# Kernel tuning notes

Measured on AMD Instinct MI355X. Metric: run time of the kernel, lower is better.

## Reference

```python
import jax, jax.numpy as jnp
import numpy as np

N = 8192          # total genes
B = 16            # number of ragged batch groups (equal-size here: 512 each)
D = 768           # hidden_dim
NEG = -1.0e9      # mask fill value used by the original module


def setup_inputs() -> dict:
    key = jax.random.key(0)
    ks = jax.random.split(key, 10)
    s = 0.02
    inp = {
        "gene_embeddings": jax.random.normal(ks[0], (N, D), dtype=jnp.float32),
        # sorted group ids: 16 contiguous groups of 512 genes
        "batch": (jnp.arange(N) // (N // B)).astype(jnp.int64),
        "Wq": jax.random.normal(ks[1], (D, D), dtype=jnp.float32) * s,
        "bq": jnp.zeros((D,), dtype=jnp.float32),
        "Wk": jax.random.normal(ks[2], (D, D), dtype=jnp.float32) * s,
        "bk": jnp.zeros((D,), dtype=jnp.float32),
        "Wv": jax.random.normal(ks[3], (D, D), dtype=jnp.float32) * s,
        "bv": jnp.zeros((D,), dtype=jnp.float32),
        "Wo": jax.random.normal(ks[4], (D, D), dtype=jnp.float32) * s,
        "bo": jnp.zeros((D,), dtype=jnp.float32),
        "beta": jnp.ones((1,), dtype=jnp.float32) * 0.1,
    }
    return inp


def reference(gene_embeddings, batch, Wq, bq, Wk, bk, Wv, bv, Wo, bo, beta):
    # Single-head attention over full hidden_dim (num_heads unused in original).
    x = gene_embeddings
    q = x @ Wq.T + bq                      # [N, D]
    k = x @ Wk.T + bk
    v = x @ Wv.T + bv
    scale = 1.0 / jnp.sqrt(jnp.asarray(D, dtype=x.dtype))
    scores = (q @ k.T) * scale             # [N, N]
    # block-diagonal group mask + diagonal self-mask (same -1e9 fill as torch code)
    same_group = batch[:, None] == batch[None, :]
    eye = jnp.eye(N, dtype=bool)
    allow = same_group & (~eye)
    scores = jnp.where(allow, scores, NEG)
    weights = jax.nn.softmax(scores, axis=-1)   # dropout in eval mode -> identity
    dyn = weights @ v                       # [N, D]
    dyn = dyn @ Wo.T + bo
    return x + beta * dyn
```

## Files before the change

kernel.cpp:

```cpp
#include <hip/hip_runtime.h>
#include <hip/hip_bf16.h>
#include <cstdint>

using u16 = unsigned short;
using u32 = unsigned int;

typedef __bf16 bf16x8 __attribute__((ext_vector_type(8)));
typedef float  f32x4  __attribute__((ext_vector_type(4)));

__device__ __forceinline__ u32 f2b2(float a, float b) {
    __hip_bfloat162 h = __float22bfloat162_rn(float2{a, b});
    u32 u;
    __builtin_memcpy(&u, &h, 4);
    return u;
}
__device__ __forceinline__ float b2f(u16 b) {
    u32 u = (u32)b << 16;
    float f;
    __builtin_memcpy(&f, &u, 4);
    return f;
}

__device__ __forceinline__ void gload_lds16(const u16* g, u16* l) {
    __builtin_amdgcn_global_load_lds(
        (const __attribute__((address_space(1))) void*)g,
        (__attribute__((address_space(3))) void*)l,
        16, 0, 0);
}

#define VMCNT(N)  asm volatile("s_waitcnt vmcnt(" #N ")" ::: "memory")
#define LGKMCNT0  asm volatile("s_waitcnt lgkmcnt(0)" ::: "memory")
#define BARRIER   asm volatile("s_barrier" ::: "memory")

__launch_bounds__(256)
__global__ void pack_kernel(const float* __restrict__ x,
                            const float* __restrict__ Wq,
                            const float* __restrict__ Wk,
                            const float* __restrict__ Wv,
                            const float* __restrict__ Wo,
                            const float* __restrict__ bq,
                            const float* __restrict__ bv,
                            const float* __restrict__ bo,
                            u16* __restrict__ xb,
                            u16* __restrict__ Wob,
                            u16* __restrict__ WqT,
                            u16* __restrict__ WkT,
                            u16* __restrict__ WvT,
                            float* __restrict__ czk,
                            float* __restrict__ bvoo)
{
    __shared__ u16 tl[64][72];
    const int b = blockIdx.x, tid = threadIdx.x;

    if (b < 3360) {
        int c = b * 256 + tid;
        long e = (long)c * 8;
        const float* src; u16* dst; long off;
        if (e < 6291456L) { src = x;  dst = xb;  off = e; }
        else              { src = Wo; dst = Wob; off = e - 6291456L; }
        float4 v0 = *(const float4*)(src + off);
        float4 v1 = *(const float4*)(src + off + 4);
        uint4 o;
        o.x = f2b2(v0.x, v0.y); o.y = f2b2(v0.z, v0.w);
        o.z = f2b2(v1.x, v1.y); o.w = f2b2(v1.z, v1.w);
        *(uint4*)(dst + off) = o;
    } else if (b < 3792) {
        int t = b - 3360;
        int w = t / 144, tt = t % 144;
        int tr = tt / 12, tc = tt % 12;
        const float* src0 = (w == 0) ? Wq : (w == 1) ? Wk : Wv;
        u16* dst0 = (w == 0) ? WqT : (w == 1) ? WkT : WvT;
        int lr = tid >> 2, lcb = (tid & 3) * 16;
        const float* src = src0 + (long)(tr * 64 + lr) * 768 + tc * 64 + lcb;
#pragma unroll
        for (int q = 0; q < 4; q++) {
            float4 v = *(const float4*)(src + q * 4);
            u32 p0 = f2b2(v.x, v.y), p1 = f2b2(v.z, v.w);
            tl[lr][lcb + q * 4 + 0] = (u16)p0;
            tl[lr][lcb + q * 4 + 1] = (u16)(p0 >> 16);
            tl[lr][lcb + q * 4 + 2] = (u16)p1;
            tl[lr][lcb + q * 4 + 3] = (u16)(p1 >> 16);
        }
        __syncthreads();
        int li = tid >> 2, lkb = (tid & 3) * 16;
        u16 o[16];
#pragma unroll
        for (int j = 0; j < 16; j++) o[j] = tl[lkb + j][li];
        u16* dst = dst0 + (long)(tc * 64 + li) * 768 + tr * 64 + lkb;
#pragma unroll
        for (int j = 0; j < 16; j++) dst[j] = o[j];
    } else if (b < 3984) {
        int wave = tid >> 6, lane = tid & 63;
        int j = (b - 3792) * 4 + wave;
        float acc = 0.f;
#pragma unroll
        for (int i = 0; i < 12; i++) {
            int rr = i * 64 + lane;
            acc += Wk[(long)rr * 768 + j] * bq[rr];
        }
#pragma unroll
        for (int d = 32; d; d >>= 1) acc += __shfl_xor(acc, d);
        if (lane == 0) czk[j] = acc;
    } else {
        int wave = tid >> 6, lane = tid & 63;
        int j = (b - 3984) * 4 + wave;
        float acc = 0.f;
#pragma unroll
        for (int i = 0; i < 12; i++) {
            int k = i * 64 + lane;
            acc += Wo[(long)j * 768 + k] * bv[k];
        }
#pragma unroll
        for (int d = 32; d; d >>= 1) acc += __shfl_xor(acc, d);
        if (lane == 0) bvoo[j] = acc + bo[j];
    }
}

template<int TM, int TN, int MODE>
__device__ __forceinline__ void gemm_body(
        const u16* __restrict__ A, int lda, long sAz,
        const u16* __restrict__ B, int ldb, long sBz,
        void* __restrict__ Cv, int ldc, long sCz,
        int K,
        const float* __restrict__ bias,
        float scale,
        u16* __restrict__ vTout)
{
    constexpr int FI = TM / 32;
    constexpr int FJ = TN / 32;
    constexpr int CA = TM / 64;
    constexpr int CB = TN / 64;

    __shared__ u16 As[2][TM * 32];
    __shared__ u16 Bs[2][TN * 32];

    const int tid  = threadIdx.x;
    const int g    = blockIdx.z;
    const u16* Ab = A + (long)g * sAz + (long)blockIdx.y * TM * lda;
    const u16* Bb = B + (long)g * sBz + (long)blockIdx.x * TN * ldb;

    const int wave = tid >> 6, lane = tid & 63;
    const int wm = (wave >> 1) * (TM / 2), wn = (wave & 1) * (TN / 2);
    const int ln15 = lane & 15, lq = lane >> 4;

    f32x4 acc[FI][FJ];
#pragma unroll
    for (int i = 0; i < FI; i++)
#pragma unroll
        for (int j = 0; j < FJ; j++)
            acc[i][j] = (f32x4){0.f, 0.f, 0.f, 0.f};

    const int srow = lane >> 2;
    const int sc   = ((lane & 3) ^ ((lane >> 4) & 3)) * 8;
    const u16* Ag[CA]; const u16* Bg[CB];
    int Al[CA], Bl[CB];
#pragma unroll
    for (int t = 0; t < CA; t++) {
        int c = wave * CA + t;
        Ag[t] = Ab + (long)(c * 16 + srow) * lda + sc;
        Al[t] = c * 512;
    }
#pragma unroll
    for (int t = 0; t < CB; t++) {
        int c = wave * CB + t;
        Bg[t] = Bb + (long)(c * 16 + srow) * ldb + sc;
        Bl[t] = c * 512;
    }

    const int foff = ln15 * 32 + ((lq ^ (ln15 >> 2)) * 8);
    const int nk = K >> 5;

#pragma unroll
    for (int t = 0; t < CA; t++) gload_lds16(Ag[t], &As[0][Al[t]]);
#pragma unroll
    for (int t = 0; t < CB; t++) gload_lds16(Bg[t], &Bs[0][Bl[t]]);

    for (int kt = 0; kt < nk; kt++) {
        const int cur = kt & 1;
        __syncthreads();
        if (kt + 1 < nk) {
            const int k0 = (kt + 1) * 32, nxt = cur ^ 1;
#pragma unroll
            for (int t = 0; t < CA; t++) gload_lds16(Ag[t] + k0, &As[nxt][Al[t]]);
#pragma unroll
            for (int t = 0; t < CB; t++) gload_lds16(Bg[t] + k0, &Bs[nxt][Bl[t]]);
        }

        bf16x8 af[FI], bfr[FJ];
#pragma unroll
        for (int i = 0; i < FI; i++)
            af[i] = *(const bf16x8*)&As[cur][(wm / 16 + i) * 512 + foff];
#pragma unroll
        for (int j = 0; j < FJ; j++)
            bfr[j] = *(const bf16x8*)&Bs[cur][(wn / 16 + j) * 512 + foff];
#pragma unroll
        for (int i = 0; i < FI; i++)
#pragma unroll
            for (int j = 0; j < FJ; j++)
                acc[i][j] = __builtin_amdgcn_mfma_f32_16x16x32_bf16(af[i], bfr[j], acc[i][j], 0, 0, 0);
    }

    const int baseRow = blockIdx.y * TM + wm;
    const int baseCol = blockIdx.x * TN + wn;

    if constexpr (MODE == 0) {
        if (baseCol < 768) {
            u16* C = (u16*)Cv;
#pragma unroll
            for (int i = 0; i < FI; i++)
#pragma unroll
                for (int j = 0; j < FJ; j++) {
                    int col = baseCol + j * 16 + ln15;
                    float bb = bias[col];
                    u32 p01 = f2b2(acc[i][j][0] + bb, acc[i][j][1] + bb);
                    u32 p23 = f2b2(acc[i][j][2] + bb, acc[i][j][3] + bb);
                    long r0 = (long)(baseRow + i * 16 + lq * 4) * ldc + col;
                    C[r0]           = (u16)p01;
                    C[r0 + ldc]     = (u16)(p01 >> 16);
                    C[r0 + 2 * ldc] = (u16)p23;
                    C[r0 + 3 * ldc] = (u16)(p23 >> 16);
                }
        } else {
#pragma unroll
            for (int i = 0; i < FI; i++)
#pragma unroll
                for (int j = 0; j < FJ; j++) {
                    int col = baseCol + j * 16 + ln15;
                    uint2 o;
                    o.x = f2b2(acc[i][j][0], acc[i][j][1]);
                    o.y = f2b2(acc[i][j][2], acc[i][j][3]);
                    *(uint2*)(vTout + (long)(col - 768) * 8192
                              + baseRow + i * 16 + lq * 4) = o;
                }
        }
    } else {
        u16* C = (u16*)Cv + (long)g * sCz;
#pragma unroll
        for (int i = 0; i < FI; i++)
#pragma unroll
            for (int j = 0; j < FJ; j++) {
                int col = baseCol + j * 16 + ln15;
                u32 p01 = f2b2(acc[i][j][0], acc[i][j][1]);
                u32 p23 = f2b2(acc[i][j][2], acc[i][j][3]);
                long r0 = (long)(baseRow + i * 16 + lq * 4) * ldc + col;
                C[r0]           = (u16)p01;
                C[r0 + ldc]     = (u16)(p01 >> 16);
                C[r0 + 2 * ldc] = (u16)p23;
                C[r0 + 3 * ldc] = (u16)(p23 >> 16);
            }
    }
}

__launch_bounds__(256)
__global__ void k_ww(const u16* WA, const u16* WB, void* WZplus)
{
    gemm_body<64, 128, 3>(WA, 768, 589824L, WB, 768, 589824L,
                          WZplus, 768, -589824L, 768,
                          nullptr, 0.f, nullptr);
}
__launch_bounds__(256)
__global__ void k_zv(const u16* A, const u16* B, void* C, const float* bias,
                     u16* vTout)
{
    gemm_body<128, 128, 0>(A, 768, 0, B, 768, 0, C, 768, 0, 768,
                           bias, 0.f, vTout);
}

__launch_bounds__(512)
__global__ void k_fattn(const u16* __restrict__ zbuf,
                        const u16* __restrict__ xb,
                        const u16* __restrict__ vwT,
                        float* __restrict__ out,
                        const float* __restrict__ bvoo,
                        const float* __restrict__ betaPtr,
                        float scale)
{
    __shared__ __align__(16) u16 smem[57344];
    u16* zl = smem;
    u16* xB = smem + 24576;
    u16* Pl = smem;
    float* redM = (float*)(smem + 16384);
    float* redS = (float*)(smem + 16896);
    u16* Vs = smem + 18432;

    const int bx = blockIdx.x;
    const int lg = ((bx & 7) << 5) + (bx >> 3);
    const int g = lg >> 4, rt = lg & 15;

    const int tid = threadIdx.x;
    const int wave = tid >> 6, lane = tid & 63;
    const int ln15 = lane & 15, lq = lane >> 4;
    const int srow = lane >> 2;
    const int sc = ((lane & 3) ^ ((lane >> 4) & 3)) * 8;
    const int foff = ln15 * 32 + ((lq ^ (ln15 >> 2)) * 8);

    const long rowBase = (long)(g * 512 + rt * 32);
    const u16* Zb = zbuf + rowBase * 768;
    const u16* Xg = xb + (long)g * 512 * 768;

#pragma unroll
    for (int n = 0; n < 6; n++) {
        int cc = n * 8 + wave;
        gload_lds16(Zb + (long)((cc & 1) * 16 + srow) * 768 + (cc >> 1) * 32 + sc,
                    &zl[cc * 512]);
    }
    const u16* xsrc[4];
#pragma unroll
    for (int c = 0; c < 4; c++)
        xsrc[c] = Xg + (long)(wave * 64 + c * 16 + srow) * 768 + sc;
    u16* xd = xB + wave * 4096;
#pragma unroll
    for (int c = 0; c < 4; c++) gload_lds16(xsrc[c], &xd[c * 512]);
#pragma unroll
    for (int c = 0; c < 4; c++) gload_lds16(xsrc[c] + 32, &xd[2048 + c * 512]);

    VMCNT(8);
    BARRIER;

    f32x4 acc[2][4];
#pragma unroll
    for (int mh = 0; mh < 2; mh++)
#pragma unroll
        for (int j = 0; j < 4; j++)
            acc[mh][j] = (f32x4){0.f, 0.f, 0.f, 0.f};

    for (int kt = 0; kt < 24; kt++) {
        const int cur = kt & 1;
        if (kt < 23) { VMCNT(4); } else { VMCNT(0); }
        bf16x8 af0 = *(const bf16x8*)&zl[(kt * 2 + 0) * 512 + foff];
        bf16x8 af1 = *(const bf16x8*)&zl[(kt * 2 + 1) * 512 + foff];
        bf16x8 bfr[4];
#pragma unroll
        for (int j = 0; j < 4; j++)
            bfr[j] = *(const bf16x8*)&xd[cur * 2048 + j * 512 + foff];
        LGKMCNT0;
        if (kt + 2 < 24) {
            const int k0 = (kt + 2) * 32;
#pragma unroll
            for (int c = 0; c < 4; c++)
                gload_lds16(xsrc[c] + k0, &xd[cur * 2048 + c * 512]);
        }
        __builtin_amdgcn_s_setprio(1);
#pragma unroll
        for (int j = 0; j < 4; j++) {
            acc[0][j] = __builtin_amdgcn_mfma_f32_16x16x32_bf16(af0, bfr[j], acc[0][j], 0, 0, 0);
            acc[1][j] = __builtin_amdgcn_mfma_f32_16x16x32_bf16(af1, bfr[j], acc[1][j], 0, 0, 0);
        }
        __builtin_amdgcn_s_setprio(0);
    }

    __syncthreads();

#pragma unroll
    for (int sub = 0; sub < 2; sub++)
        gload_lds16(vwT + (long)(wave * 16 + srow) * 8192 + g * 512 + sub * 32 + sc,
                    &Vs[sub * 4096 + wave * 512]);
#pragma unroll
    for (int sub = 0; sub < 2; sub++)
        gload_lds16(vwT + (long)(wave * 16 + srow) * 8192 + g * 512 + 64 + sub * 32 + sc,
                    &Vs[8192 + sub * 4096 + wave * 512]);

    float mx[2][4];
#pragma unroll
    for (int mh = 0; mh < 2; mh++)
#pragma unroll
        for (int rr = 0; rr < 4; rr++) mx[mh][rr] = -3.0e38f;
#pragma unroll
    for (int mh = 0; mh < 2; mh++)
#pragma unroll
        for (int j = 0; j < 4; j++)
#pragma unroll
            for (int rr = 0; rr < 4; rr++) {
                const int col = wave * 64 + j * 16 + ln15;
                float v = acc[mh][j][rr] * scale;
                if (rt * 32 + mh * 16 + lq * 4 + rr == col) v = -1.0e9f;
                acc[mh][j][rr] = v;
                mx[mh][rr] = fmaxf(mx[mh][rr], v);
            }
#pragma unroll
    for (int mh = 0; mh < 2; mh++)
#pragma unroll
        for (int rr = 0; rr < 4; rr++) {
            mx[mh][rr] = fmaxf(mx[mh][rr], __shfl_xor(mx[mh][rr], 1));
            mx[mh][rr] = fmaxf(mx[mh][rr], __shfl_xor(mx[mh][rr], 2));
            mx[mh][rr] = fmaxf(mx[mh][rr], __shfl_xor(mx[mh][rr], 4));
            mx[mh][rr] = fmaxf(mx[mh][rr], __shfl_xor(mx[mh][rr], 8));
        }
    if (ln15 == 0) {
#pragma unroll
        for (int mh = 0; mh < 2; mh++)
#pragma unroll
            for (int rr = 0; rr < 4; rr++)
                redM[(mh * 16 + lq * 4 + rr) * 8 + wave] = mx[mh][rr];
    }
    __syncthreads();

    float m_[2][4], s_[2][4];
#pragma unroll
    for (int mh = 0; mh < 2; mh++)
#pragma unroll
        for (int rr = 0; rr < 4; rr++) {
            const int row = mh * 16 + lq * 4 + rr;
            float4 a = *(const float4*)&redM[row * 8];
            float4 b = *(const float4*)&redM[row * 8 + 4];
            m_[mh][rr] = fmaxf(fmaxf(fmaxf(a.x, a.y), fmaxf(a.z, a.w)),
                               fmaxf(fmaxf(b.x, b.y), fmaxf(b.z, b.w)));
            s_[mh][rr] = 0.f;
        }
#pragma unroll
    for (int mh = 0; mh < 2; mh++)
#pragma unroll
        for (int j = 0; j < 4; j++)
#pragma unroll
            for (int rr = 0; rr < 4; rr++) {
                float p = __expf(acc[mh][j][rr] - m_[mh][rr]);
                acc[mh][j][rr] = p;
                s_[mh][rr] += p;
            }
#pragma unroll
    for (int mh = 0; mh < 2; mh++)
#pragma unroll
        for (int rr = 0; rr < 4; rr++) {
            s_[mh][rr] += __shfl_xor(s_[mh][rr], 1);
            s_[mh][rr] += __shfl_xor(s_[mh][rr], 2);
            s_[mh][rr] += __shfl_xor(s_[mh][rr], 4);
            s_[mh][rr] += __shfl_xor(s_[mh][rr], 8);
        }
    if (ln15 == 0) {
#pragma unroll
        for (int mh = 0; mh < 2; mh++)
#pragma unroll
            for (int rr = 0; rr < 4; rr++)
                redS[(mh * 16 + lq * 4 + rr) * 8 + wave] = s_[mh][rr];
    }
#pragma unroll
    for (int mh = 0; mh < 2; mh++)
#pragma unroll
        for (int j = 0; j < 4; j++) {
            const int col = wave * 64 + j * 16 + ln15;
            const int c8 = col >> 3, b7 = col & 7;
#pragma unroll
            for (int rr = 0; rr < 4; rr++) {
                const int row = mh * 16 + lq * 4 + rr;
                Pl[(row * 64 + (c8 ^ (row & 7))) * 8 + b7] =
                    (u16)f2b2(acc[mh][j][rr], acc[mh][j][rr]);
            }
        }
    __syncthreads();

    const int wm3 = (wave >> 2) * 16;
    const int wnP = (wave & 3) * 32;
    float invS[4];
#pragma unroll
    for (int rr = 0; rr < 4; rr++) {
        const int row = wm3 + lq * 4 + rr;
        float4 a = *(const float4*)&redS[row * 8];
        float4 b = *(const float4*)&redS[row * 8 + 4];
        invS[rr] = 1.0f / (a.x + a.y + a.z + a.w + b.x + b.y + b.z + b.w);
    }
    const int prow = wm3 + ln15;
    bf16x8 apr[16];
#pragma unroll
    for (int k4 = 0; k4 < 16; k4++)
        apr[k4] = *(const bf16x8*)&Pl[(prow * 64 + ((k4 * 4 + lq) ^ (prow & 7))) * 8];

    f32x4 aP[6][2];
#pragma unroll
    for (int ct = 0; ct < 6; ct++) {
        aP[ct][0] = (f32x4){0.f, 0.f, 0.f, 0.f};
        aP[ct][1] = (f32x4){0.f, 0.f, 0.f, 0.f};
    }

#pragma unroll
    for (int ct = 0; ct < 6; ct++) {
#pragma unroll
        for (int kk = 0; kk < 8; kk++) {
            const int ts = ct * 8 + kk;
            const int cur = ts % 3;
            if (ts < 47) { VMCNT(2); } else { VMCNT(0); }
            BARRIER;
            bf16x8 b0[2], b1[2];
#pragma unroll
            for (int sub = 0; sub < 2; sub++) {
                b0[sub] = *(const bf16x8*)&Vs[cur * 8192 + sub * 4096
                                              + (wnP >> 4) * 512 + foff];
                b1[sub] = *(const bf16x8*)&Vs[cur * 8192 + sub * 4096
                                              + ((wnP >> 4) + 1) * 512 + foff];
            }
            if (ts + 2 < 48) {
                const int tn = ts + 2, ctn = tn >> 3, kkn = tn & 7;
                const int nb = tn % 3;
#pragma unroll
                for (int sub = 0; sub < 2; sub++)
                    gload_lds16(vwT + (long)(ctn * 128 + wave * 16 + srow) * 8192
                                    + g * 512 + kkn * 64 + sub * 32 + sc,
                                &Vs[nb * 8192 + sub * 4096 + wave * 512]);
            }
            __builtin_amdgcn_s_setprio(1);
#pragma unroll
            for (int sub = 0; sub < 2; sub++) {
                aP[ct][0] = __builtin_amdgcn_mfma_f32_16x16x32_bf16(apr[kk * 2 + sub], b0[sub], aP[ct][0], 0, 0, 0);
                aP[ct][1] = __builtin_amdgcn_mfma_f32_16x16x32_bf16(apr[kk * 2 + sub], b1[sub], aP[ct][1], 0, 0, 0);
            }
            __builtin_amdgcn_s_setprio(0);
        }
    }

    const float bet = betaPtr[0];
    const u16* Xr = xb + (rowBase + wm3 + lq * 4) * 768;
    float* O = out + (rowBase + wm3 + lq * 4) * 768;
#pragma unroll
    for (int ct = 0; ct < 6; ct++) {
#pragma unroll
        for (int jj = 0; jj < 2; jj++) {
            const int col = ct * 128 + wnP + jj * 16 + ln15;
            const float bb = bvoo[col];
#pragma unroll
            for (int rr = 0; rr < 4; rr++)
                O[rr * 768 + col] = b2f(Xr[rr * 768 + col])
                                    + bet * (invS[rr] * aP[ct][jj][rr] + bb);
        }
    }
}

extern "C" void kernel_launch(void* const* d_in, const int* in_sizes, int n_in,
                              void* d_out, int out_size, void* d_ws, size_t ws_size,
                              hipStream_t stream)
{
    const float* x    = (const float*)d_in[0];
    const float* Wq   = (const float*)d_in[2];
    const float* bq   = (const float*)d_in[3];
    const float* Wk   = (const float*)d_in[4];
    const float* bk   = (const float*)d_in[5];
    const float* Wv   = (const float*)d_in[6];
    const float* bv   = (const float*)d_in[7];
    const float* Wo   = (const float*)d_in[8];
    const float* bo   = (const float*)d_in[9];
    const float* beta = (const float*)d_in[10];
    float* out = (float*)d_out;
    (void)bk;

    char* ws = (char*)d_ws;
    u16*   zbuf = (u16*)(ws + 0);
    u16*   vwT  = (u16*)(ws + 12582912);
    u16*   xb   = (u16*)(ws + 25165824);
    u16*   WA   = (u16*)(ws + 46137344);
    u16*   WB   = (u16*)(ws + 48496640);
    u16*   WZ   = (u16*)(ws + 50855936);
    float* czk  = (float*)(ws + 53215232);
    float* bvoo = (float*)(ws + 53218304);

    u16* Wob = WA;
    u16* WkT = WA + 589824;
    u16* WvT = WB;
    u16* WqT = WB + 589824;

    const float scale = 0.03608439182435161f;

    pack_kernel<<<4176, 256, 0, stream>>>(x, Wq, Wk, Wv, Wo, bq, bv, bo,
                                          xb, Wob, WqT, WkT, WvT, czk, bvoo);

    k_ww<<<dim3(6, 12, 2), 256, 0, stream>>>(WA, WB, (void*)(WZ + 589824L));

    k_zv<<<dim3(12, 64, 1), 256, 0, stream>>>(xb, WZ, (void*)zbuf, czk, vwT);

    k_fattn<<<dim3(256), 512, 0, stream>>>(zbuf, xb, vwT, out, bvoo, beta,
                                           scale);
}
```

Measured before the change: 187.1 us.

## Double fused-attention block to 1024 threads and re-split work across 16 waves

The fused attention kernel now launches 1024 threads (16 waves) per block instead of 512. Each wave computes half as many score columns and a single 16-column slice of the PV output, and reads P fragments from LDS inside the loop instead of preloading 16 of them into registers. The goal is more waves in flight per block to hide latency and lower per-thread register pressure. The cost is more barrier participants, more repeated LDS reads of P, and smaller MFMA batches per wave.

```diff
diff --git a/kernel.cpp b/kernel.cpp
--- a/kernel.cpp
+++ b/kernel.cpp
@@ -266,7 +266,7 @@
                            bias, 0.f, vTout);
 }
 
-__launch_bounds__(512)
+__launch_bounds__(1024, 4)
 __global__ void k_fattn(const u16* __restrict__ zbuf,
                         const u16* __restrict__ xb,
                         const u16* __restrict__ vwT,
@@ -277,10 +277,10 @@
 {
     __shared__ __align__(16) u16 smem[57344];
     u16* zl = smem;
-    u16* xB = smem + 24576;
+    u16* xS = smem + 24576;
     u16* Pl = smem;
     float* redM = (float*)(smem + 16384);
-    float* redS = (float*)(smem + 16896);
+    float* redS = (float*)(smem + 17408);
     u16* Vs = smem + 18432;
 
     const int bx = blockIdx.x;
@@ -299,50 +299,50 @@
     const u16* Xg = xb + (long)g * 512 * 768;
 
 #pragma unroll
-    for (int n = 0; n < 6; n++) {
-        int cc = n * 8 + wave;
+    for (int n = 0; n < 3; n++) {
+        int cc = n * 16 + wave;
         gload_lds16(Zb + (long)((cc & 1) * 16 + srow) * 768 + (cc >> 1) * 32 + sc,
                     &zl[cc * 512]);
     }
-    const u16* xsrc[4];
-#pragma unroll
-    for (int c = 0; c < 4; c++)
-        xsrc[c] = Xg + (long)(wave * 64 + c * 16 + srow) * 768 + sc;
-    u16* xd = xB + wave * 4096;
-#pragma unroll
-    for (int c = 0; c < 4; c++) gload_lds16(xsrc[c], &xd[c * 512]);
-#pragma unroll
-    for (int c = 0; c < 4; c++) gload_lds16(xsrc[c] + 32, &xd[2048 + c * 512]);
-
-    VMCNT(8);
+    const u16* xsrc[2];
+#pragma unroll
+    for (int c = 0; c < 2; c++)
+        xsrc[c] = Xg + (long)(wave * 32 + c * 16 + srow) * 768 + sc;
+    u16* xd = xS + wave * 2048;
+#pragma unroll
+    for (int c = 0; c < 2; c++) gload_lds16(xsrc[c], &xd[c * 512]);
+#pragma unroll
+    for (int c = 0; c < 2; c++) gload_lds16(xsrc[c] + 32, &xd[1024 + c * 512]);
+
+    VMCNT(4);
     BARRIER;
 
-    f32x4 acc[2][4];
-#pragma unroll
-    for (int mh = 0; mh < 2; mh++)
-#pragma unroll
-        for (int j = 0; j < 4; j++)
+    f32x4 acc[2][2];
+#pragma unroll
+    for (int mh = 0; mh < 2; mh++)
+#pragma unroll
+        for (int j = 0; j < 2; j++)
             acc[mh][j] = (f32x4){0.f, 0.f, 0.f, 0.f};
 
     for (int kt = 0; kt < 24; kt++) {
         const int cur = kt & 1;
-        if (kt < 23) { VMCNT(4); } else { VMCNT(0); }
+        if (kt < 23) { VMCNT(2); } else { VMCNT(0); }
         bf16x8 af0 = *(const bf16x8*)&zl[(kt * 2 + 0) * 512 + foff];
         bf16x8 af1 = *(const bf16x8*)&zl[(kt * 2 + 1) * 512 + foff];
-        bf16x8 bfr[4];
-#pragma unroll
-        for (int j = 0; j < 4; j++)
-            bfr[j] = *(const bf16x8*)&xd[cur * 2048 + j * 512 + foff];
+        bf16x8 bfr[2];
+#pragma unroll
+        for (int j = 0; j < 2; j++)
+            bfr[j] = *(const bf16x8*)&xd[cur * 1024 + j * 512 + foff];
         LGKMCNT0;
         if (kt + 2 < 24) {
             const int k0 = (kt + 2) * 32;
 #pragma unroll
-            for (int c = 0; c < 4; c++)
-                gload_lds16(xsrc[c] + k0, &xd[cur * 2048 + c * 512]);
+            for (int c = 0; c < 2; c++)
+                gload_lds16(xsrc[c] + k0, &xd[cur * 1024 + c * 512]);
         }
         __builtin_amdgcn_s_setprio(1);
 #pragma unroll
-        for (int j = 0; j < 4; j++) {
+        for (int j = 0; j < 2; j++) {
             acc[0][j] = __builtin_amdgcn_mfma_f32_16x16x32_bf16(af0, bfr[j], acc[0][j], 0, 0, 0);
             acc[1][j] = __builtin_amdgcn_mfma_f32_16x16x32_bf16(af1, bfr[j], acc[1][j], 0, 0, 0);
         }
@@ -351,14 +351,14 @@
 
     __syncthreads();
 
-#pragma unroll
-    for (int sub = 0; sub < 2; sub++)
-        gload_lds16(vwT + (long)(wave * 16 + srow) * 8192 + g * 512 + sub * 32 + sc,
-                    &Vs[sub * 4096 + wave * 512]);
-#pragma unroll
-    for (int sub = 0; sub < 2; sub++)
-        gload_lds16(vwT + (long)(wave * 16 + srow) * 8192 + g * 512 + 64 + sub * 32 + sc,
-                    &Vs[8192 + sub * 4096 + wave * 512]);
+    {
+        const int cw = wave & 7, sh = wave >> 3;
+#pragma unroll
+        for (int ts = 0; ts < 2; ts++)
+            gload_lds16(vwT + (long)(0 * 128 + cw * 16 + srow) * 8192
+                            + g * 512 + ts * 64 + sh * 32 + sc,
+                        &Vs[ts * 8192 + cw * 1024 + sh * 512]);
+    }
 
     float mx[2][4];
 #pragma unroll
@@ -368,10 +368,10 @@
 #pragma unroll
     for (int mh = 0; mh < 2; mh++)
 #pragma unroll
-        for (int j = 0; j < 4; j++)
+        for (int j = 0; j < 2; j++)
 #pragma unroll
             for (int rr = 0; rr < 4; rr++) {
-                const int col = wave * 64 + j * 16 + ln15;
+                const int col = wave * 32 + j * 16 + ln15;
                 float v = acc[mh][j][rr] * scale;
                 if (rt * 32 + mh * 16 + lq * 4 + rr == col) v = -1.0e9f;
                 acc[mh][j][rr] = v;
@@ -391,7 +391,7 @@
         for (int mh = 0; mh < 2; mh++)
 #pragma unroll
             for (int rr = 0; rr < 4; rr++)
-                redM[(mh * 16 + lq * 4 + rr) * 8 + wave] = mx[mh][rr];
+                redM[(mh * 16 + lq * 4 + rr) * 16 + wave] = mx[mh][rr];
     }
     __syncthreads();
 
@@ -401,16 +401,19 @@
 #pragma unroll
         for (int rr = 0; rr < 4; rr++) {
             const int row = mh * 16 + lq * 4 + rr;
-            float4 a = *(const float4*)&redM[row * 8];
-            float4 b = *(const float4*)&redM[row * 8 + 4];
-            m_[mh][rr] = fmaxf(fmaxf(fmaxf(a.x, a.y), fmaxf(a.z, a.w)),
-                               fmaxf(fmaxf(b.x, b.y), fmaxf(b.z, b.w)));
+            float mm = -3.0e38f;
+#pragma unroll
+            for (int q = 0; q < 4; q++) {
+                float4 a = *(const float4*)&redM[row * 16 + q * 4];
+                mm = fmaxf(mm, fmaxf(fmaxf(a.x, a.y), fmaxf(a.z, a.w)));
+            }
+            m_[mh][rr] = mm;
             s_[mh][rr] = 0.f;
         }
 #pragma unroll
     for (int mh = 0; mh < 2; mh++)
 #pragma unroll
-        for (int j = 0; j < 4; j++)
+        for (int j = 0; j < 2; j++)
 #pragma unroll
             for (int rr = 0; rr < 4; rr++) {
                 float p = __expf(acc[mh][j][rr] - m_[mh][rr]);
@@ -431,13 +434,13 @@
         for (int mh = 0; mh < 2; mh++)
 #pragma unroll
             for (int rr = 0; rr < 4; rr++)
-                redS[(mh * 16 + lq * 4 + rr) * 8 + wave] = s_[mh][rr];
-    }
-#pragma unroll
-    for (int mh = 0; mh < 2; mh++)
-#pragma unroll
-        for (int j = 0; j < 4; j++) {
-            const int col = wave * 64 + j * 16 + ln15;
+                redS[(mh * 16 + lq * 4 + rr) * 16 + wave] = s_[mh][rr];
+    }
+#pragma unroll
+    for (int mh = 0; mh < 2; mh++)
+#pragma unroll
+        for (int j = 0; j < 2; j++) {
+            const int col = wave * 32 + j * 16 + ln15;
             const int c8 = col >> 3, b7 = col & 7;
 #pragma unroll
             for (int rr = 0; rr < 4; rr++) {
@@ -448,28 +451,26 @@
         }
     __syncthreads();
 
-    const int wm3 = (wave >> 2) * 16;
-    const int wnP = (wave & 3) * 32;
+    const int wm3 = (wave >> 3) * 16;
+    const int cw  = wave & 7;
+    const int sh  = wave >> 3;
+    const int prow = wm3 + ln15;
     float invS[4];
 #pragma unroll
     for (int rr = 0; rr < 4; rr++) {
         const int row = wm3 + lq * 4 + rr;
-        float4 a = *(const float4*)&redS[row * 8];
-        float4 b = *(const float4*)&redS[row * 8 + 4];
-        invS[rr] = 1.0f / (a.x + a.y + a.z + a.w + b.x + b.y + b.z + b.w);
-    }
-    const int prow = wm3 + ln15;
-    bf16x8 apr[16];
-#pragma unroll
-    for (int k4 = 0; k4 < 16; k4++)
-        apr[k4] = *(const bf16x8*)&Pl[(prow * 64 + ((k4 * 4 + lq) ^ (prow & 7))) * 8];
-
-    f32x4 aP[6][2];
-#pragma unroll
-    for (int ct = 0; ct < 6; ct++) {
-        aP[ct][0] = (f32x4){0.f, 0.f, 0.f, 0.f};
-        aP[ct][1] = (f32x4){0.f, 0.f, 0.f, 0.f};
-    }
+        float ss = 0.f;
+#pragma unroll
+        for (int q = 0; q < 4; q++) {
+            float4 a = *(const float4*)&redS[row * 16 + q * 4];
+            ss += a.x + a.y + a.z + a.w;
+        }
+        invS[rr] = 1.0f / ss;
+    }
+
+    f32x4 aP[6];
+#pragma unroll
+    for (int ct = 0; ct < 6; ct++) aP[ct] = (f32x4){0.f, 0.f, 0.f, 0.f};
 
 #pragma unroll
     for (int ct = 0; ct < 6; ct++) {
@@ -477,31 +478,29 @@
         for (int kk = 0; kk < 8; kk++) {
             const int ts = ct * 8 + kk;
             const int cur = ts % 3;
-            if (ts < 47) { VMCNT(2); } else { VMCNT(0); }
+            if (ts < 47) { VMCNT(1); } else { VMCNT(0); }
             BARRIER;
-            bf16x8 b0[2], b1[2];
+            bf16x8 pa[2], bv_[2];
 #pragma unroll
             for (int sub = 0; sub < 2; sub++) {
-                b0[sub] = *(const bf16x8*)&Vs[cur * 8192 + sub * 4096
-                                              + (wnP >> 4) * 512 + foff];
-                b1[sub] = *(const bf16x8*)&Vs[cur * 8192 + sub * 4096
-                                              + ((wnP >> 4) + 1) * 512 + foff];
-            }
+                pa[sub]  = *(const bf16x8*)&Pl[(prow * 64
+                              + (((kk * 2 + sub) * 4 + lq) ^ (prow & 7))) * 8];
+                bv_[sub] = *(const bf16x8*)&Vs[cur * 8192 + cw * 1024
+                                               + sub * 512 + foff];
+            }
+            LGKMCNT0;
+            __builtin_amdgcn_sched_barrier(0);
             if (ts + 2 < 48) {
                 const int tn = ts + 2, ctn = tn >> 3, kkn = tn & 7;
                 const int nb = tn % 3;
-#pragma unroll
-                for (int sub = 0; sub < 2; sub++)
-                    gload_lds16(vwT + (long)(ctn * 128 + wave * 16 + srow) * 8192
-                                    + g * 512 + kkn * 64 + sub * 32 + sc,
-                                &Vs[nb * 8192 + sub * 4096 + wave * 512]);
+                gload_lds16(vwT + (long)(ctn * 128 + cw * 16 + srow) * 8192
+                                + g * 512 + kkn * 64 + sh * 32 + sc,
+                            &Vs[nb * 8192 + cw * 1024 + sh * 512]);
             }
             __builtin_amdgcn_s_setprio(1);
 #pragma unroll
-            for (int sub = 0; sub < 2; sub++) {
-                aP[ct][0] = __builtin_amdgcn_mfma_f32_16x16x32_bf16(apr[kk * 2 + sub], b0[sub], aP[ct][0], 0, 0, 0);
-                aP[ct][1] = __builtin_amdgcn_mfma_f32_16x16x32_bf16(apr[kk * 2 + sub], b1[sub], aP[ct][1], 0, 0, 0);
-            }
+            for (int sub = 0; sub < 2; sub++)
+                aP[ct] = __builtin_amdgcn_mfma_f32_16x16x32_bf16(pa[sub], bv_[sub], aP[ct], 0, 0, 0);
             __builtin_amdgcn_s_setprio(0);
         }
     }
@@ -511,15 +510,12 @@
     float* O = out + (rowBase + wm3 + lq * 4) * 768;
 #pragma unroll
     for (int ct = 0; ct < 6; ct++) {
-#pragma unroll
-        for (int jj = 0; jj < 2; jj++) {
-            const int col = ct * 128 + wnP + jj * 16 + ln15;
-            const float bb = bvoo[col];
-#pragma unroll
-            for (int rr = 0; rr < 4; rr++)
-                O[rr * 768 + col] = b2f(Xr[rr * 768 + col])
-                                    + bet * (invS[rr] * aP[ct][jj][rr] + bb);
-        }
+        const int col = ct * 128 + cw * 16 + ln15;
+        const float bb = bvoo[col];
+#pragma unroll
+        for (int rr = 0; rr < 4; rr++)
+            O[rr * 768 + col] = b2f(Xr[rr * 768 + col])
+                                + bet * (invS[rr] * aP[ct][rr] + bb);
     }
 }
 
@@ -564,6 +560,6 @@
 
     k_zv<<<dim3(12, 64, 1), 256, 0, stream>>>(xb, WZ, (void*)zbuf, czk, vwT);
 
-    k_fattn<<<dim3(256), 512, 0, stream>>>(zbuf, xb, vwT, out, bvoo, beta,
-                                           scale);
-}
+    k_fattn<<<dim3(256), 1024, 0, stream>>>(zbuf, xb, vwT, out, bvoo, beta,
+                                            scale);
+}
```

Result: slower. 195.8 us (+4.6%).
